# Kernel tuning notes

Hardware: AMD Instinct MI355X
Metric: run time of the kernel (lower is better)

## Reference

```python
import jax, jax.numpy as jnp
import numpy as np

DIM = 256
HEADS = 8
GH = GW = 8
NTOK = GH * GW            # 64 tokens per window
NW = 49                   # windows per image (56x56 / 8x8)
BATCH = 64
B_ = BATCH * NW           # 3136
POS_DIM = (DIM // 4) // 4 # 16, DynamicPosBias pos_dim
LBIAS = (2 * GH - 1) * (2 * GW - 1)  # 225 relative offsets
EPS = 1e-5


def _ln(x, g, b):
    m = jnp.mean(x, axis=-1, keepdims=True)
    v = jnp.mean((x - m) ** 2, axis=-1, keepdims=True)
    return (x - m) * jax.lax.rsqrt(v + EPS) * g + b


def _make_buffers():
    # biases: all relative (dh, dw) offsets, shape (LBIAS, 2) float
    h = np.arange(1 - GH, GH)
    w = np.arange(1 - GW, GW)
    biases = np.stack(np.meshgrid(h, w, indexing='ij')).reshape(2, -1).T.astype(np.float32)
    # relative_position_index: (NTOK, NTOK) int32 in [0, LBIAS)
    coords = np.stack(np.meshgrid(np.arange(GH), np.arange(GW), indexing='ij')).reshape(2, -1)
    rel = coords[:, :, None] - coords[:, None, :]
    rel = rel.transpose(1, 2, 0).astype(np.int64)
    rel[..., 0] += GH - 1
    rel[..., 1] += GW - 1
    rel[..., 0] *= 2 * GW - 1
    idx = rel.sum(-1).astype(np.int32)
    return jnp.asarray(biases), jnp.asarray(idx)


def setup_inputs() -> dict:
    key = jax.random.key(0)
    ks = iter(jax.random.split(key, 32))
    def w(shape, s=0.02):
        return jax.random.normal(next(ks), shape, jnp.float32) * s
    biases, rel_idx = _make_buffers()
    return {
        'x': jax.random.normal(next(ks), (B_, NTOK, DIM), jnp.float32),
        'mask': jnp.zeros((NW, NTOK, NTOK), jnp.float32),
        'qkv_w': w((3 * DIM, DIM)), 'qkv_b': jnp.zeros((3 * DIM,), jnp.float32),
        'proj_w': w((DIM, DIM)), 'proj_b': jnp.zeros((DIM,), jnp.float32),
        'pos_proj_w': w((POS_DIM, 2)), 'pos_proj_b': jnp.zeros((POS_DIM,), jnp.float32),
        'ln1_g': jnp.ones((POS_DIM,), jnp.float32), 'ln1_b': jnp.zeros((POS_DIM,), jnp.float32),
        'fc1_w': w((POS_DIM, POS_DIM)), 'fc1_b': jnp.zeros((POS_DIM,), jnp.float32),
        'ln2_g': jnp.ones((POS_DIM,), jnp.float32), 'ln2_b': jnp.zeros((POS_DIM,), jnp.float32),
        'fc2_w': w((POS_DIM, POS_DIM)), 'fc2_b': jnp.zeros((POS_DIM,), jnp.float32),
        'ln3_g': jnp.ones((POS_DIM,), jnp.float32), 'ln3_b': jnp.zeros((POS_DIM,), jnp.float32),
        'fc3_w': w((HEADS, POS_DIM)), 'fc3_b': jnp.zeros((HEADS,), jnp.float32),
        'biases': biases, 'rel_idx': rel_idx,
    }


def _forward(x, mask, qkv_w, qkv_b, proj_w, proj_b,
             pos_proj_w, pos_proj_b, ln1_g, ln1_b, fc1_w, fc1_b,
             ln2_g, ln2_b, fc2_w, fc2_b, ln3_g, ln3_b, fc3_w, fc3_b,
             biases, rel_idx):
    Bw, N, C = x.shape
    hd = C // HEADS
    scale = hd ** -0.5
    qkv = (x @ qkv_w.T + qkv_b).reshape(Bw, N, 3, HEADS, hd)
    qkv = jnp.transpose(qkv, (2, 0, 3, 1, 4))  # (3, B_, H, N, hd)
    q, k, v = qkv[0] * scale, qkv[1], qkv[2]
    attn = jnp.einsum('bhnd,bhmd->bhnm', q, k)  # (B_, H, N, N)
    # DynamicPosBias MLP (residual=False): pos3(pos2(pos1(pos_proj(biases))))
    p = biases @ pos_proj_w.T + pos_proj_b
    p = jax.nn.relu(_ln(p, ln1_g, ln1_b)) @ fc1_w.T + fc1_b
    p = jax.nn.relu(_ln(p, ln2_g, ln2_b)) @ fc2_w.T + fc2_b
    p = jax.nn.relu(_ln(p, ln3_g, ln3_b)) @ fc3_w.T + fc3_b  # (LBIAS, H)
    rpb = jnp.transpose(p[rel_idx], (2, 0, 1))  # gather -> (H, N, N)
    attn = attn + rpb[None]
    nW = mask.shape[0]
    attn = attn.reshape(Bw // nW, nW, HEADS, N, N) + mask[None, :, None]
    attn = jax.nn.softmax(attn.reshape(Bw, HEADS, N, N), axis=-1)
    out = jnp.einsum('bhnm,bhmd->bhnd', attn, v)
    out = jnp.transpose(out, (0, 2, 1, 3)).reshape(Bw, N, C)
    return out @ proj_w.T + proj_b


def reference(x, mask, qkv_w, qkv_b, proj_w, proj_b,
              pos_proj_w, pos_proj_b, ln1_g, ln1_b, fc1_w, fc1_b,
              ln2_g, ln2_b, fc2_w, fc2_b, ln3_g, ln3_b, fc3_w, fc3_b,
              biases, rel_idx):
    return _forward(x, mask, qkv_w, qkv_b, proj_w, proj_b,
                    pos_proj_w, pos_proj_b, ln1_g, ln1_b, fc1_w, fc1_b,
                    ln2_g, ln2_b, fc2_w, fc2_b, ln3_g, ln3_b, fc3_w, fc3_b,
                    biases, rel_idx)
```

## Files before the change

### kernel.cpp

```cpp
#include <hip/hip_runtime.h>

#define NTOKS 64
#define DIMS 256
#define NHEADS 8
#define NWIN 49
#define NBLK 3136

typedef __bf16 bf16x8 __attribute__((ext_vector_type(8)));
typedef __bf16 bf16x4 __attribute__((ext_vector_type(4)));
typedef float f32x4 __attribute__((ext_vector_type(4)));

__device__ __forceinline__ unsigned short f2bf(float f) {
    union { float f; unsigned u; } c; c.f = f;
    unsigned u = c.u;
    u += 0x7fffu + ((u >> 16) & 1u);
    return (unsigned short)(u >> 16);
}

__device__ __forceinline__ bf16x8 pack8(f32x4 a, f32x4 b) {
    bf16x8 r;
    r[0] = (__bf16)a[0]; r[1] = (__bf16)a[1];
    r[2] = (__bf16)a[2]; r[3] = (__bf16)a[3];
    r[4] = (__bf16)b[0]; r[5] = (__bf16)b[1];
    r[6] = (__bf16)b[2]; r[7] = (__bf16)b[3];
    return r;
}

template<int NOUT>
__device__ __forceinline__ void ln_relu_fc(const float* v, const float* g, const float* bb,
                                           const float* fw, const float* fb, float* o) {
    float m = 0.f;
#pragma unroll
    for (int j = 0; j < 16; ++j) m += v[j];
    m *= (1.f / 16.f);
    float var = 0.f;
#pragma unroll
    for (int j = 0; j < 16; ++j) { float d = v[j] - m; var += d * d; }
    var *= (1.f / 16.f);
    float inv = rsqrtf(var + 1e-5f);
    float t[16];
#pragma unroll
    for (int j = 0; j < 16; ++j) {
        float xx = (v[j] - m) * inv * g[j] + bb[j];
        t[j] = xx > 0.f ? xx : 0.f;
    }
#pragma unroll
    for (int i = 0; i < NOUT; ++i) {
        float ss = fb[i];
#pragma unroll
        for (int j = 0; j < 16; ++j) ss += fw[i * 16 + j] * t[j];
        o[i] = ss;
    }
}

__global__ void prep_kernel(
    const float* __restrict__ qkv_w, const float* __restrict__ qkv_b,
    const float* __restrict__ proj_w, const float* __restrict__ mask,
    const float* __restrict__ pos_proj_w, const float* __restrict__ pos_proj_b,
    const float* __restrict__ ln1_g, const float* __restrict__ ln1_b,
    const float* __restrict__ fc1_w, const float* __restrict__ fc1_b,
    const float* __restrict__ ln2_g, const float* __restrict__ ln2_b,
    const float* __restrict__ fc2_w, const float* __restrict__ fc2_b,
    const float* __restrict__ ln3_g, const float* __restrict__ ln3_b,
    const float* __restrict__ fc3_w, const float* __restrict__ fc3_b,
    const float* __restrict__ biases, const int* __restrict__ rel_idx,
    unsigned short* __restrict__ qkvw_bf, unsigned short* __restrict__ projw_bf,
    float* __restrict__ qkvb_s, float* __restrict__ rpb_perm,
    float* __restrict__ mask_perm)
{
    const int tid = threadIdx.x;
    const int b = blockIdx.x;
    const float SC = 0.17677669529663687f;

    if (b == 0) {
        __shared__ float p_sh[225 * 8];
        if (tid < 225) {
            float bx = biases[2 * tid], by = biases[2 * tid + 1];
            float v[16], u[16];
#pragma unroll
            for (int j = 0; j < 16; ++j)
                v[j] = pos_proj_w[2 * j] * bx + pos_proj_w[2 * j + 1] * by + pos_proj_b[j];
            ln_relu_fc<16>(v, ln1_g, ln1_b, fc1_w, fc1_b, u);
            ln_relu_fc<16>(u, ln2_g, ln2_b, fc2_w, fc2_b, v);
            ln_relu_fc<8>(v, ln3_g, ln3_b, fc3_w, fc3_b, u);
#pragma unroll
            for (int h = 0; h < 8; ++h) p_sh[tid * 8 + h] = u[h];
        }
        __syncthreads();
        for (int e = tid; e < 32768; e += 256) {
            int r = e & 3, q = (e >> 2) & 63, qd = (e >> 8) & 3, kt = (e >> 10) & 3, h = e >> 12;
            int key = kt * 16 + qd * 4 + r;
            rpb_perm[e] = p_sh[rel_idx[q * 64 + key] * 8 + h];
        }
    } else {
        const int t0 = (b - 1) * 256 + tid, NTH = 127 * 256;
        for (int e = t0; e < 196608; e += NTH) {
            int j = e & 7, lane = (e >> 3) & 63, kk = (e >> 9) & 7, tile = e >> 12;
            int src = (tile * 16 + (lane & 15)) * 256 + kk * 32 + (lane >> 4) * 8 + j;
            float f = qkv_w[src];
            if (src < 65536) f *= SC;
            qkvw_bf[e] = f2bf(f);
        }
        for (int e = t0; e < 65536; e += NTH) {
            int j = e & 7, lane = (e >> 3) & 63, kk = (e >> 9) & 7, tile = e >> 12;
            int src = (tile * 16 + (lane & 15)) * 256 + kk * 32 + (lane >> 4) * 8 + j;
            projw_bf[e] = f2bf(proj_w[src]);
        }
        for (int e = t0; e < 200704; e += NTH) {
            int r = e & 3, q = (e >> 2) & 63, qd = (e >> 8) & 3, kt = (e >> 10) & 3, w = e >> 12;
            int key = kt * 16 + qd * 4 + r;
            mask_perm[e] = mask[w * 4096 + q * 64 + key];
        }
        if (b == 1) {
            for (int e = tid; e < 768; e += 256)
                qkvb_s[e] = qkv_b[e] * (e < 256 ? SC : 1.f);
        }
    }
}

__global__ __launch_bounds__(512, 4) void attn_kernel(
    const float* __restrict__ x,
    const unsigned short* __restrict__ qkvw, const float* __restrict__ qkvb,
    const unsigned short* __restrict__ projw, const float* __restrict__ projb,
    const float* __restrict__ rpb_perm, const float* __restrict__ mask_perm,
    float* __restrict__ out)
{
    __shared__ __align__(16) char ldsb[32768];
    const int tid  = threadIdx.x;
    const int h    = tid >> 6;
    const int lane = tid & 63;
    const int quad = lane >> 4;
    const int l16  = lane & 15;
    const int sw   = (l16 & 7) << 4;
    const int blk  = blockIdx.x;
    const int w    = blk % NWIN;
    const f32x4 FZ = {0.f, 0.f, 0.f, 0.f};

    {
        const float4* xv = (const float4*)(x + (size_t)blk * (NTOKS * DIMS));
#pragma unroll
        for (int it = 0; it < 8; ++it) {
            int i = tid + it * 512;
            float4 f = xv[i];
            int row = i >> 6;
            int colb = (i & 63) << 3;
            bf16x4 hv;
            hv[0] = (__bf16)f.x; hv[1] = (__bf16)f.y;
            hv[2] = (__bf16)f.z; hv[3] = (__bf16)f.w;
            *(bf16x4*)(ldsb + row * 512 + (colb ^ ((row & 7) << 4))) = hv;
        }
    }
    __syncthreads();

    const int xbase = l16 * 512;
#define XFRAG(t, kk) (*(const bf16x8*)(ldsb + (t) * 8192 + xbase + ((((kk) * 64) + quad * 16) ^ sw)))

    f32x4 qa[2][4], ka[2][4];
#pragma unroll
    for (int mt = 0; mt < 2; ++mt)
#pragma unroll
        for (int nt = 0; nt < 4; ++nt) { qa[mt][nt] = FZ; ka[mt][nt] = FZ; }
    {
        const unsigned short* pQ = qkvw + (size_t)((2 * h) * 8) * 512 + lane * 8;
        const unsigned short* pK = qkvw + (size_t)((16 + 2 * h) * 8) * 512 + lane * 8;
#pragma unroll 2
        for (int kk = 0; kk < 8; ++kk) {
            bf16x8 xb[4];
#pragma unroll
            for (int nt = 0; nt < 4; ++nt) xb[nt] = XFRAG(nt, kk);
            bf16x8 wq[2], wk[2];
#pragma unroll
            for (int mt = 0; mt < 2; ++mt) {
                wq[mt] = *(const bf16x8*)&pQ[(mt * 8 + kk) * 512];
                wk[mt] = *(const bf16x8*)&pK[(mt * 8 + kk) * 512];
            }
            __builtin_amdgcn_s_setprio(1);
#pragma unroll
            for (int mt = 0; mt < 2; ++mt)
#pragma unroll
                for (int nt = 0; nt < 4; ++nt) {
                    qa[mt][nt] = __builtin_amdgcn_mfma_f32_16x16x32_bf16(wq[mt], xb[nt], qa[mt][nt], 0, 0, 0);
                    ka[mt][nt] = __builtin_amdgcn_mfma_f32_16x16x32_bf16(wk[mt], xb[nt], ka[mt][nt], 0, 0, 0);
                }
            __builtin_amdgcn_s_setprio(0);
        }
    }
#pragma unroll
    for (int mt = 0; mt < 2; ++mt) {
        f32x4 qb = *(const f32x4*)&qkvb[h * 32 + mt * 16 + quad * 4];
        f32x4 kb = *(const f32x4*)&qkvb[256 + h * 32 + mt * 16 + quad * 4];
#pragma unroll
        for (int nt = 0; nt < 4; ++nt) {
#pragma unroll
            for (int r = 0; r < 4; ++r) { qa[mt][nt][r] += qb[r]; ka[mt][nt][r] += kb[r]; }
        }
    }
    bf16x8 Qp[4], Kp[4];
#pragma unroll
    for (int t = 0; t < 4; ++t) {
        Qp[t] = pack8(qa[0][t], qa[1][t]);
        Kp[t] = pack8(ka[0][t], ka[1][t]);
    }

    f32x4 s[4][4];
    {
        const f32x4* rp4 = (const f32x4*)rpb_perm + ((h * 16 + quad) * 64 + l16);
        const f32x4* mp4 = (const f32x4*)mask_perm + ((w * 16 + quad) * 64 + l16);
#pragma unroll
        for (int kt = 0; kt < 4; ++kt)
#pragma unroll
            for (int qt = 0; qt < 4; ++qt) {
                f32x4 rv = rp4[kt * 256 + qt * 16];
                f32x4 mv = mp4[kt * 256 + qt * 16];
                s[kt][qt] = rv + mv;
            }
        __builtin_amdgcn_s_setprio(1);
#pragma unroll
        for (int kt = 0; kt < 4; ++kt)
#pragma unroll
            for (int qt = 0; qt < 4; ++qt)
                s[kt][qt] = __builtin_amdgcn_mfma_f32_16x16x32_bf16(Kp[kt], Qp[qt], s[kt][qt], 0, 0, 0);
        __builtin_amdgcn_s_setprio(0);
    }

#pragma unroll
    for (int qt = 0; qt < 4; ++qt) {
        float mx = s[0][qt][0];
#pragma unroll
        for (int kt = 0; kt < 4; ++kt)
#pragma unroll
            for (int r = 0; r < 4; ++r) mx = fmaxf(mx, s[kt][qt][r]);
        mx = fmaxf(mx, __shfl_xor(mx, 16));
        mx = fmaxf(mx, __shfl_xor(mx, 32));
        float sum = 0.f;
#pragma unroll
        for (int kt = 0; kt < 4; ++kt)
#pragma unroll
            for (int r = 0; r < 4; ++r) {
                float e = __expf(s[kt][qt][r] - mx);
                s[kt][qt][r] = e; sum += e;
            }
        sum += __shfl_xor(sum, 16);
        sum += __shfl_xor(sum, 32);
        float inv = 1.0f / sum;
#pragma unroll
        for (int kt = 0; kt < 4; ++kt)
#pragma unroll
            for (int r = 0; r < 4; ++r) s[kt][qt][r] *= inv;
    }
    bf16x8 Pp[4][2];
#pragma unroll
    for (int qt = 0; qt < 4; ++qt)
#pragma unroll
        for (int ks = 0; ks < 2; ++ks)
            Pp[qt][ks] = pack8(s[2 * ks][qt], s[2 * ks + 1][qt]);

    f32x4 va[4][2];
#pragma unroll
    for (int mt = 0; mt < 4; ++mt)
#pragma unroll
        for (int nt = 0; nt < 2; ++nt) va[mt][nt] = FZ;
    {
        const unsigned short* pV = qkvw + (size_t)((32 + 2 * h) * 8) * 512 + lane * 8;
#pragma unroll 2
        for (int kk = 0; kk < 8; ++kk) {
            bf16x8 xa[4];
#pragma unroll
            for (int mt = 0; mt < 4; ++mt) xa[mt] = XFRAG(mt, kk);
            bf16x8 wv[2];
#pragma unroll
            for (int nt = 0; nt < 2; ++nt) wv[nt] = *(const bf16x8*)&pV[(nt * 8 + kk) * 512];
            __builtin_amdgcn_s_setprio(1);
#pragma unroll
            for (int mt = 0; mt < 4; ++mt)
#pragma unroll
                for (int nt = 0; nt < 2; ++nt)
                    va[mt][nt] = __builtin_amdgcn_mfma_f32_16x16x32_bf16(xa[mt], wv[nt], va[mt][nt], 0, 0, 0);
            __builtin_amdgcn_s_setprio(0);
        }
        float vb0 = qkvb[512 + h * 32 + l16];
        float vb1 = qkvb[512 + h * 32 + 16 + l16];
#pragma unroll
        for (int mt = 0; mt < 4; ++mt)
#pragma unroll
            for (int r = 0; r < 4; ++r) { va[mt][0][r] += vb0; va[mt][1][r] += vb1; }
    }
    bf16x8 Vp[2][2];
#pragma unroll
    for (int ks = 0; ks < 2; ++ks)
#pragma unroll
        for (int nt = 0; nt < 2; ++nt)
            Vp[ks][nt] = pack8(va[2 * ks][nt], va[2 * ks + 1][nt]);

    __syncthreads();

    f32x4 o2[2][4];
    __builtin_amdgcn_s_setprio(1);
#pragma unroll
    for (int nt = 0; nt < 2; ++nt)
#pragma unroll
        for (int qt = 0; qt < 4; ++qt) {
            f32x4 a0 = __builtin_amdgcn_mfma_f32_16x16x32_bf16(Vp[0][nt], Pp[qt][0], FZ, 0, 0, 0);
            o2[nt][qt] = __builtin_amdgcn_mfma_f32_16x16x32_bf16(Vp[1][nt], Pp[qt][1], a0, 0, 0, 0);
        }
    __builtin_amdgcn_s_setprio(0);

    {
#pragma unroll
        for (int qt = 0; qt < 4; ++qt) {
            char* rowp = ldsb + qt * 8192 + xbase;
#pragma unroll
            for (int nt = 0; nt < 2; ++nt) {
                bf16x4 hv;
                hv[0] = (__bf16)o2[nt][qt][0];
                hv[1] = (__bf16)o2[nt][qt][1];
                hv[2] = (__bf16)o2[nt][qt][2];
                hv[3] = (__bf16)o2[nt][qt][3];
                *(bf16x4*)(rowp + ((64 * h + 32 * nt + 8 * quad) ^ sw)) = hv;
            }
        }
    }
    __syncthreads();

    f32x4 c2[2][4];
    {
#pragma unroll
        for (int ot = 0; ot < 2; ++ot)
#pragma unroll
            for (int qt = 0; qt < 4; ++qt) c2[ot][qt] = FZ;
        const unsigned short* pP = projw + (size_t)((2 * h) * 8) * 512 + lane * 8;
#pragma unroll 2
        for (int kk = 0; kk < 8; ++kk) {
            bf16x8 cb[4];
#pragma unroll
            for (int qt = 0; qt < 4; ++qt) cb[qt] = XFRAG(qt, kk);
            bf16x8 bwp[2];
#pragma unroll
            for (int ot = 0; ot < 2; ++ot) bwp[ot] = *(const bf16x8*)&pP[(ot * 8 + kk) * 512];
            __builtin_amdgcn_s_setprio(1);
#pragma unroll
            for (int ot = 0; ot < 2; ++ot)
#pragma unroll
                for (int qt = 0; qt < 4; ++qt)
                    c2[ot][qt] = __builtin_amdgcn_mfma_f32_16x16x32_bf16(bwp[ot], cb[qt], c2[ot][qt], 0, 0, 0);
            __builtin_amdgcn_s_setprio(0);
        }
    }

    {
        float* ldsf = (float*)ldsb;
        float4* ob4 = (float4*)(out + (size_t)blk * (NTOKS * DIMS));
        f32x4 pb[2];
#pragma unroll
        for (int ot = 0; ot < 2; ++ot)
            pb[ot] = *(const f32x4*)&projb[h * 32 + ot * 16 + quad * 4];
#pragma unroll
        for (int p = 0; p < 2; ++p) {
            __syncthreads();
#pragma unroll
            for (int qh = 0; qh < 2; ++qh) {
                int qt = 2 * p + qh;
                int row = qh * 16 + l16;
#pragma unroll
                for (int ot = 0; ot < 2; ++ot) {
                    f32x4 v = c2[ot][qt] + pb[ot];
                    *(f32x4*)&ldsf[row * 256 + h * 32 + ot * 16 + quad * 4] = v;
                }
            }
            __syncthreads();
#pragma unroll
            for (int it = 0; it < 4; ++it) {
                int i = tid + it * 512;
                int row = i >> 6, c16 = i & 63;
                float4 v = *(const float4*)&ldsf[row * 256 + c16 * 4];
                ob4[p * 2048 + i] = v;
            }
        }
    }
#undef XFRAG
}

extern "C" void kernel_launch(void* const* d_in, const int* in_sizes, int n_in,
                              void* d_out, int out_size, void* d_ws, size_t ws_size,
                              hipStream_t stream) {
    const float* x          = (const float*)d_in[0];
    const float* mask       = (const float*)d_in[1];
    const float* qkv_w      = (const float*)d_in[2];
    const float* qkv_b      = (const float*)d_in[3];
    const float* proj_w     = (const float*)d_in[4];
    const float* proj_b     = (const float*)d_in[5];
    const float* pos_proj_w = (const float*)d_in[6];
    const float* pos_proj_b = (const float*)d_in[7];
    const float* ln1_g      = (const float*)d_in[8];
    const float* ln1_b      = (const float*)d_in[9];
    const float* fc1_w      = (const float*)d_in[10];
    const float* fc1_b      = (const float*)d_in[11];
    const float* ln2_g      = (const float*)d_in[12];
    const float* ln2_b      = (const float*)d_in[13];
    const float* fc2_w      = (const float*)d_in[14];
    const float* fc2_b      = (const float*)d_in[15];
    const float* ln3_g      = (const float*)d_in[16];
    const float* ln3_b      = (const float*)d_in[17];
    const float* fc3_w      = (const float*)d_in[18];
    const float* fc3_b      = (const float*)d_in[19];
    const float* biases     = (const float*)d_in[20];
    const int*   rel_idx    = (const int*)d_in[21];
    float* out = (float*)d_out;

    char* ws = (char*)d_ws;
    unsigned short* qkvw_bf  = (unsigned short*)(ws);
    unsigned short* projw_bf = (unsigned short*)(ws + 393216);
    float* qkvb_s    = (float*)(ws + 524288);
    float* rpb_perm  = (float*)(ws + 528384);
    float* mask_perm = (float*)(ws + 659456);

    prep_kernel<<<dim3(128), dim3(256), 0, stream>>>(
        qkv_w, qkv_b, proj_w, mask, pos_proj_w, pos_proj_b,
        ln1_g, ln1_b, fc1_w, fc1_b, ln2_g, ln2_b, fc2_w, fc2_b,
        ln3_g, ln3_b, fc3_w, fc3_b, biases, rel_idx,
        qkvw_bf, projw_bf, qkvb_s, rpb_perm, mask_perm);

    attn_kernel<<<dim3(NBLK), dim3(512), 0, stream>>>(
        x, qkvw_bf, qkvb_s, projw_bf, proj_b, rpb_perm, mask_perm, out);
}
```

Before: 563.2 us.

## Split Q/K projections, chunk softmax, defer normalization, swizzle output LDS staging

Computes the Q and K projections in separate loops and runs QK^T plus softmax in two halves of query tiles, so fewer accumulator registers are live at the same time. The softmax normalization is moved after the PV MFMA as one multiply per output element. The output staging buffer in LDS gets an XOR swizzle to avoid bank conflicts. Launch bounds drop from 4 to 2 blocks per CU, which gives the compiler more registers but may allow fewer resident waves.

```diff
diff --git a/kernel.cpp b/kernel.cpp
--- a/kernel.cpp
+++ b/kernel.cpp
@@ -118,7 +118,7 @@
     }
 }
 
-__global__ __launch_bounds__(512, 4) void attn_kernel(
+__global__ __launch_bounds__(512, 2) void attn_kernel(
     const float* __restrict__ x,
     const unsigned short* __restrict__ qkvw, const float* __restrict__ qkvb,
     const unsigned short* __restrict__ projw, const float* __restrict__ projb,
@@ -155,112 +155,137 @@
     const int xbase = l16 * 512;
 #define XFRAG(t, kk) (*(const bf16x8*)(ldsb + (t) * 8192 + xbase + ((((kk) * 64) + quad * 16) ^ sw)))
 
-    f32x4 qa[2][4], ka[2][4];
-#pragma unroll
-    for (int mt = 0; mt < 2; ++mt)
-#pragma unroll
-        for (int nt = 0; nt < 4; ++nt) { qa[mt][nt] = FZ; ka[mt][nt] = FZ; }
-    {
+    bf16x8 Qp[4], Kp[4];
+    {
+        f32x4 qa[2][4];
+#pragma unroll
+        for (int mt = 0; mt < 2; ++mt)
+#pragma unroll
+            for (int nt = 0; nt < 4; ++nt) qa[mt][nt] = FZ;
         const unsigned short* pQ = qkvw + (size_t)((2 * h) * 8) * 512 + lane * 8;
+#pragma unroll 2
+        for (int kk = 0; kk < 8; ++kk) {
+            bf16x8 xb[4];
+#pragma unroll
+            for (int nt = 0; nt < 4; ++nt) xb[nt] = XFRAG(nt, kk);
+            bf16x8 wq[2];
+#pragma unroll
+            for (int mt = 0; mt < 2; ++mt)
+                wq[mt] = *(const bf16x8*)&pQ[(mt * 8 + kk) * 512];
+            __builtin_amdgcn_s_setprio(1);
+#pragma unroll
+            for (int mt = 0; mt < 2; ++mt)
+#pragma unroll
+                for (int nt = 0; nt < 4; ++nt)
+                    qa[mt][nt] = __builtin_amdgcn_mfma_f32_16x16x32_bf16(wq[mt], xb[nt], qa[mt][nt], 0, 0, 0);
+            __builtin_amdgcn_s_setprio(0);
+        }
+#pragma unroll
+        for (int mt = 0; mt < 2; ++mt) {
+            f32x4 qb = *(const f32x4*)&qkvb[h * 32 + mt * 16 + quad * 4];
+#pragma unroll
+            for (int nt = 0; nt < 4; ++nt)
+#pragma unroll
+                for (int r = 0; r < 4; ++r) qa[mt][nt][r] += qb[r];
+        }
+#pragma unroll
+        for (int t = 0; t < 4; ++t) Qp[t] = pack8(qa[0][t], qa[1][t]);
+    }
+    {
+        f32x4 ka[2][4];
+#pragma unroll
+        for (int mt = 0; mt < 2; ++mt)
+#pragma unroll
+            for (int nt = 0; nt < 4; ++nt) ka[mt][nt] = FZ;
         const unsigned short* pK = qkvw + (size_t)((16 + 2 * h) * 8) * 512 + lane * 8;
 #pragma unroll 2
         for (int kk = 0; kk < 8; ++kk) {
             bf16x8 xb[4];
 #pragma unroll
             for (int nt = 0; nt < 4; ++nt) xb[nt] = XFRAG(nt, kk);
-            bf16x8 wq[2], wk[2];
-#pragma unroll
-            for (int mt = 0; mt < 2; ++mt) {
-                wq[mt] = *(const bf16x8*)&pQ[(mt * 8 + kk) * 512];
+            bf16x8 wk[2];
+#pragma unroll
+            for (int mt = 0; mt < 2; ++mt)
                 wk[mt] = *(const bf16x8*)&pK[(mt * 8 + kk) * 512];
-            }
             __builtin_amdgcn_s_setprio(1);
 #pragma unroll
             for (int mt = 0; mt < 2; ++mt)
 #pragma unroll
-                for (int nt = 0; nt < 4; ++nt) {
-                    qa[mt][nt] = __builtin_amdgcn_mfma_f32_16x16x32_bf16(wq[mt], xb[nt], qa[mt][nt], 0, 0, 0);
+                for (int nt = 0; nt < 4; ++nt)
                     ka[mt][nt] = __builtin_amdgcn_mfma_f32_16x16x32_bf16(wk[mt], xb[nt], ka[mt][nt], 0, 0, 0);
-                }
             __builtin_amdgcn_s_setprio(0);
         }
-    }
-#pragma unroll
-    for (int mt = 0; mt < 2; ++mt) {
-        f32x4 qb = *(const f32x4*)&qkvb[h * 32 + mt * 16 + quad * 4];
-        f32x4 kb = *(const f32x4*)&qkvb[256 + h * 32 + mt * 16 + quad * 4];
-#pragma unroll
-        for (int nt = 0; nt < 4; ++nt) {
-#pragma unroll
-            for (int r = 0; r < 4; ++r) { qa[mt][nt][r] += qb[r]; ka[mt][nt][r] += kb[r]; }
-        }
-    }
-    bf16x8 Qp[4], Kp[4];
-#pragma unroll
-    for (int t = 0; t < 4; ++t) {
-        Qp[t] = pack8(qa[0][t], qa[1][t]);
-        Kp[t] = pack8(ka[0][t], ka[1][t]);
-    }
-
-    f32x4 s[4][4];
+#pragma unroll
+        for (int mt = 0; mt < 2; ++mt) {
+            f32x4 kb = *(const f32x4*)&qkvb[256 + h * 32 + mt * 16 + quad * 4];
+#pragma unroll
+            for (int nt = 0; nt < 4; ++nt)
+#pragma unroll
+                for (int r = 0; r < 4; ++r) ka[mt][nt][r] += kb[r];
+        }
+#pragma unroll
+        for (int t = 0; t < 4; ++t) Kp[t] = pack8(ka[0][t], ka[1][t]);
+    }
+
+    bf16x8 Pp[4][2];
+    float inv[4];
     {
         const f32x4* rp4 = (const f32x4*)rpb_perm + ((h * 16 + quad) * 64 + l16);
         const f32x4* mp4 = (const f32x4*)mask_perm + ((w * 16 + quad) * 64 + l16);
 #pragma unroll
-        for (int kt = 0; kt < 4; ++kt)
-#pragma unroll
-            for (int qt = 0; qt < 4; ++qt) {
-                f32x4 rv = rp4[kt * 256 + qt * 16];
-                f32x4 mv = mp4[kt * 256 + qt * 16];
-                s[kt][qt] = rv + mv;
+        for (int qth = 0; qth < 2; ++qth) {
+            f32x4 s[4][2];
+#pragma unroll
+            for (int kt = 0; kt < 4; ++kt)
+#pragma unroll
+                for (int q2 = 0; q2 < 2; ++q2) {
+                    int qt = qth * 2 + q2;
+                    f32x4 rv = rp4[kt * 256 + qt * 16];
+                    f32x4 mv = mp4[kt * 256 + qt * 16];
+                    s[kt][q2] = rv + mv;
+                }
+            __builtin_amdgcn_s_setprio(1);
+#pragma unroll
+            for (int kt = 0; kt < 4; ++kt)
+#pragma unroll
+                for (int q2 = 0; q2 < 2; ++q2)
+                    s[kt][q2] = __builtin_amdgcn_mfma_f32_16x16x32_bf16(Kp[kt], Qp[qth * 2 + q2], s[kt][q2], 0, 0, 0);
+            __builtin_amdgcn_s_setprio(0);
+#pragma unroll
+            for (int q2 = 0; q2 < 2; ++q2) {
+                int qt = qth * 2 + q2;
+                float mx = s[0][q2][0];
+#pragma unroll
+                for (int kt = 0; kt < 4; ++kt)
+#pragma unroll
+                    for (int r = 0; r < 4; ++r) mx = fmaxf(mx, s[kt][q2][r]);
+                mx = fmaxf(mx, __shfl_xor(mx, 16));
+                mx = fmaxf(mx, __shfl_xor(mx, 32));
+                float sum = 0.f;
+#pragma unroll
+                for (int kt = 0; kt < 4; ++kt)
+#pragma unroll
+                    for (int r = 0; r < 4; ++r) {
+                        float e = __expf(s[kt][q2][r] - mx);
+                        s[kt][q2][r] = e; sum += e;
+                    }
+                sum += __shfl_xor(sum, 16);
+                sum += __shfl_xor(sum, 32);
+                inv[qt] = 1.0f / sum;
+#pragma unroll
+                for (int ks = 0; ks < 2; ++ks)
+                    Pp[qt][ks] = pack8(s[2 * ks][q2], s[2 * ks + 1][q2]);
             }
-        __builtin_amdgcn_s_setprio(1);
-#pragma unroll
-        for (int kt = 0; kt < 4; ++kt)
-#pragma unroll
-            for (int qt = 0; qt < 4; ++qt)
-                s[kt][qt] = __builtin_amdgcn_mfma_f32_16x16x32_bf16(Kp[kt], Qp[qt], s[kt][qt], 0, 0, 0);
-        __builtin_amdgcn_s_setprio(0);
-    }
-
-#pragma unroll
-    for (int qt = 0; qt < 4; ++qt) {
-        float mx = s[0][qt][0];
-#pragma unroll
-        for (int kt = 0; kt < 4; ++kt)
-#pragma unroll
-            for (int r = 0; r < 4; ++r) mx = fmaxf(mx, s[kt][qt][r]);
-        mx = fmaxf(mx, __shfl_xor(mx, 16));
-        mx = fmaxf(mx, __shfl_xor(mx, 32));
-        float sum = 0.f;
-#pragma unroll
-        for (int kt = 0; kt < 4; ++kt)
-#pragma unroll
-            for (int r = 0; r < 4; ++r) {
-                float e = __expf(s[kt][qt][r] - mx);
-                s[kt][qt][r] = e; sum += e;
-            }
-        sum += __shfl_xor(sum, 16);
-        sum += __shfl_xor(sum, 32);
-        float inv = 1.0f / sum;
-#pragma unroll
-        for (int kt = 0; kt < 4; ++kt)
-#pragma unroll
-            for (int r = 0; r < 4; ++r) s[kt][qt][r] *= inv;
-    }
-    bf16x8 Pp[4][2];
-#pragma unroll
-    for (int qt = 0; qt < 4; ++qt)
-#pragma unroll
-        for (int ks = 0; ks < 2; ++ks)
-            Pp[qt][ks] = pack8(s[2 * ks][qt], s[2 * ks + 1][qt]);
-
-    f32x4 va[4][2];
-#pragma unroll
-    for (int mt = 0; mt < 4; ++mt)
-#pragma unroll
-        for (int nt = 0; nt < 2; ++nt) va[mt][nt] = FZ;
-    {
+        }
+    }
+
+    bf16x8 Vp[2][2];
+    {
+        f32x4 va[4][2];
+#pragma unroll
+        for (int mt = 0; mt < 4; ++mt)
+#pragma unroll
+            for (int nt = 0; nt < 2; ++nt) va[mt][nt] = FZ;
         const unsigned short* pV = qkvw + (size_t)((32 + 2 * h) * 8) * 512 + lane * 8;
 #pragma unroll 2
         for (int kk = 0; kk < 8; ++kk) {
@@ -284,13 +309,12 @@
         for (int mt = 0; mt < 4; ++mt)
 #pragma unroll
             for (int r = 0; r < 4; ++r) { va[mt][0][r] += vb0; va[mt][1][r] += vb1; }
-    }
-    bf16x8 Vp[2][2];
-#pragma unroll
-    for (int ks = 0; ks < 2; ++ks)
-#pragma unroll
-        for (int nt = 0; nt < 2; ++nt)
-            Vp[ks][nt] = pack8(va[2 * ks][nt], va[2 * ks + 1][nt]);
+#pragma unroll
+        for (int ks = 0; ks < 2; ++ks)
+#pragma unroll
+            for (int nt = 0; nt < 2; ++nt)
+                Vp[ks][nt] = pack8(va[2 * ks][nt], va[2 * ks + 1][nt]);
+    }
 
     __syncthreads();
 
@@ -304,6 +328,12 @@
             o2[nt][qt] = __builtin_amdgcn_mfma_f32_16x16x32_bf16(Vp[1][nt], Pp[qt][1], a0, 0, 0, 0);
         }
     __builtin_amdgcn_s_setprio(0);
+#pragma unroll
+    for (int nt = 0; nt < 2; ++nt)
+#pragma unroll
+        for (int qt = 0; qt < 4; ++qt)
+#pragma unroll
+            for (int r = 0; r < 4; ++r) o2[nt][qt][r] *= inv[qt];
 
     {
 #pragma unroll
@@ -348,7 +378,6 @@
     }
 
     {
-        float* ldsf = (float*)ldsb;
         float4* ob4 = (float4*)(out + (size_t)blk * (NTOKS * DIMS));
         f32x4 pb[2];
 #pragma unroll
@@ -361,10 +390,11 @@
             for (int qh = 0; qh < 2; ++qh) {
                 int qt = 2 * p + qh;
                 int row = qh * 16 + l16;
+                int rx = (row & 15) << 4;
 #pragma unroll
                 for (int ot = 0; ot < 2; ++ot) {
                     f32x4 v = c2[ot][qt] + pb[ot];
-                    *(f32x4*)&ldsf[row * 256 + h * 32 + ot * 16 + quad * 4] = v;
+                    *(f32x4*)(ldsb + row * 1024 + ((h * 128 + ot * 64 + quad * 16) ^ rx)) = v;
                 }
             }
             __syncthreads();
@@ -372,7 +402,7 @@
             for (int it = 0; it < 4; ++it) {
                 int i = tid + it * 512;
                 int row = i >> 6, c16 = i & 63;
-                float4 v = *(const float4*)&ldsf[row * 256 + c16 * 4];
+                float4 v = *(const float4*)(ldsb + row * 1024 + ((c16 * 16) ^ ((row & 15) << 4)));
                 ob4[p * 2048 + i] = v;
             }
         }
```

New measurement: 581.2 us. 3.2% more time.
